# Kernel tuning notes

Hardware: AMD Instinct MI355X
Metric: run time of the kernel (lower is better)

Reference implementation:

```python
import jax, jax.numpy as jnp
import numpy as np

EMB = 1024
HEADS = 8
SEQ = 4096
LN_EPS = 1e-5


def _layernorm(x, g, b):
    mu = jnp.mean(x, axis=-1, keepdims=True)
    var = jnp.mean(jnp.square(x - mu), axis=-1, keepdims=True)
    return (x - mu) * jax.lax.rsqrt(var + LN_EPS) * g + b


def setup_inputs() -> dict:
    key = jax.random.key(0)
    ks = jax.random.split(key, 12)
    s = 1.0 / np.sqrt(EMB)
    sz = 1.0 / np.sqrt(EMB * HEADS)
    return {
        "history": jax.random.normal(ks[0], (SEQ, EMB), jnp.float32),
        "embdding": jax.random.normal(ks[1], (SEQ, EMB), jnp.float32),
        # per-head Linear weights, torch layout [out, in], stacked over heads
        "Wq_w": jax.random.uniform(ks[2], (HEADS, EMB, EMB), jnp.float32, -s, s),
        "Wq_b": jax.random.uniform(ks[3], (HEADS, EMB), jnp.float32, -s, s),
        "Wk_w": jax.random.uniform(ks[4], (HEADS, EMB, EMB), jnp.float32, -s, s),
        "Wk_b": jax.random.uniform(ks[5], (HEADS, EMB), jnp.float32, -s, s),
        "Wv_w": jax.random.uniform(ks[6], (HEADS, EMB, EMB), jnp.float32, -s, s),
        "Wv_b": jax.random.uniform(ks[7], (HEADS, EMB), jnp.float32, -s, s),
        "Wz_w": jax.random.uniform(ks[8], (EMB, EMB * HEADS), jnp.float32, -sz, sz),
        "Wz_b": jax.random.uniform(ks[9], (EMB,), jnp.float32, -sz, sz),
        "ln1_g": jnp.ones((EMB,), jnp.float32),
        "ln1_b": jnp.zeros((EMB,), jnp.float32),
        "Wf_w": jax.random.uniform(ks[10], (EMB, EMB), jnp.float32, -s, s),
        "Wf_b": jax.random.uniform(ks[11], (EMB,), jnp.float32, -s, s),
        "ln2_g": jnp.ones((EMB,), jnp.float32),
        "ln2_b": jnp.zeros((EMB,), jnp.float32),
    }


def reference(history, embdding, Wq_w, Wq_b, Wk_w, Wk_b, Wv_w, Wv_b,
              Wz_w, Wz_b, ln1_g, ln1_b, Wf_w, Wf_b, ln2_g, ln2_b):
    S, E = embdding.shape
    H = Wq_w.shape[0]
    # per-head linears (torch: y = x @ W.T + b), batched over heads
    Q = jnp.einsum('se,hfe->hsf', embdding, Wq_w) + Wq_b[:, None, :]  # [H,S,E]
    K = jnp.einsum('se,hfe->hsf', embdding, Wk_w) + Wk_b[:, None, :]
    V = jnp.einsum('se,hfe->hsf', history, Wv_w) + Wv_b[:, None, :]
    # K^T @ Q -> [H, E, E], softmax over dim=1 of the 2D matrix == last axis here
    scores = jnp.einsum('hse,hsf->hef', K, Q) / jnp.sqrt(jnp.asarray(E, Q.dtype))
    A = jax.nn.softmax(scores, axis=-1)  # [H,E,E]
    Zh = jnp.einsum('hse,hef->hsf', V, A)  # [H,S,E]
    Z = jnp.transpose(Zh, (1, 0, 2)).reshape(S, H * E)  # cat(dim=1) in head order
    O = Z @ Wz_w.T + Wz_b  # [S,E]
    LN1 = _layernorm(O, ln1_g, ln1_b) + embdding
    FN = LN1 @ Wf_w.T + Wf_b
    LN2 = _layernorm(FN, ln2_g, ln2_b) + LN1
    return LN2
```

## Files before the change

kernel.cpp:

```cpp
#include <hip/hip_runtime.h>


constexpr int EMB = 1024;
constexpr int SEQ = 4096;
constexpr int NH  = 8;

using f32x4  = __attribute__((ext_vector_type(4))) float;
using bf16x8 = __attribute__((ext_vector_type(8))) __bf16;
using us8    = __attribute__((ext_vector_type(8))) unsigned short;
using us4    = __attribute__((ext_vector_type(4))) unsigned short;

#define GLOAD_LDS16(g, l) __builtin_amdgcn_global_load_lds(                 \
    (const __attribute__((address_space(1))) void*)(g),                     \
    (__attribute__((address_space(3))) void*)(l), 16, 0, 0)

__device__ inline unsigned short f2bf(float x) {
  unsigned int u = __float_as_uint(x);
  u += 0x7FFFu + ((u >> 16) & 1u);
  return (unsigned short)(u >> 16);
}
__device__ inline float bf2f(unsigned short h) {
  return __uint_as_float(((unsigned int)h) << 16);
}
__device__ inline f32x4 ntl4(const float* p) {
  return __builtin_nontemporal_load((const f32x4*)p);
}
__device__ inline us4 cvt4(f32x4 x) {
  us4 o; o[0] = f2bf(x[0]); o[1] = f2bf(x[1]); o[2] = f2bf(x[2]); o[3] = f2bf(x[3]);
  return o;
}

template <int MODE>
__device__ __attribute__((always_inline)) void gemm_body(
    unsigned short* lds, int bx, int by, int z,
    const unsigned short* A, const unsigned short* B, void* Cout,
    int K, int lda, int ldb, int ldc,
    long long aZ, long long bZ, long long cZ,
    const float* e0, const float* e1, const float* e2, const float* e3,
    float* mpart, float* spart) {
  A += (size_t)z * aZ;
  B += (size_t)z * bZ;
  const int tid = threadIdx.x;
  const int lane = tid & 63, wid = tid >> 6;
  const int wm = wid >> 1, wn = wid & 1;
  const int row0 = bx * 64, col0 = by * 128;

  unsigned short* As = lds;
  unsigned short* Bs = lds + 64 * 64;

  f32x4 acc[2][4] = {};
  const int lrow = lane & 15, kg = lane >> 4;
  const int lr = lane >> 3;
  const int lc = (lane & 7) * 8;

  const int nt = K >> 6;
  for (int t = 0; t < nt; ++t) {
    const int k0 = t << 6;
#pragma unroll
    for (int c = 0; c < 2; ++c) {
      int chunk = wid * 2 + c;
      int r = chunk * 8 + lr;
      GLOAD_LDS16(A + (size_t)(row0 + r) * lda + k0 + lc, &As[chunk * 512]);
    }
#pragma unroll
    for (int c = 0; c < 4; ++c) {
      int chunk = wid * 4 + c;
      int r = chunk * 8 + lr;
      GLOAD_LDS16(B + (size_t)(col0 + r) * ldb + k0 + lc, &Bs[chunk * 512]);
    }
    __syncthreads();
#pragma unroll
    for (int ks = 0; ks < 2; ++ks) {
      bf16x8 a[2], b[4];
      int koff = ks * 32 + kg * 8;
#pragma unroll
      for (int i = 0; i < 2; ++i)
        a[i] = *(const bf16x8*)&As[(wm * 32 + i * 16 + lrow) * 64 + koff];
#pragma unroll
      for (int j = 0; j < 4; ++j)
        b[j] = *(const bf16x8*)&Bs[(wn * 64 + j * 16 + lrow) * 64 + koff];
#pragma unroll
      for (int i = 0; i < 2; ++i)
#pragma unroll
        for (int j = 0; j < 4; ++j)
          acc[i][j] = __builtin_amdgcn_mfma_f32_16x16x32_bf16(a[i], b[j], acc[i][j], 0, 0, 0);
    }
    __syncthreads();
  }

  const int rb = (lane >> 4) * 4, cc = lane & 15;
  unsigned short* Cs = lds;
#pragma unroll
  for (int i = 0; i < 2; ++i) {
#pragma unroll
    for (int j = 0; j < 4; ++j) {
#pragma unroll
      for (int r = 0; r < 4; ++r) {
        float val = acc[i][j][r];
        int mm = wm * 32 + i * 16 + rb + r;
        int nn = wn * 64 + j * 16 + cc;
        if (MODE == 4) {
          int m = row0 + mm, n = col0 + nn;
          float bq = e0[z * EMB + m], uu = e1[z * EMB + n];
          float bk = e2[z * EMB + n], vv = e3[z * EMB + m];
          val = (val + bq * (uu + (float)SEQ * bk) + vv * bk) * (1.0f / 32.0f);
        } else if (MODE == 5) {
          val += e0[col0 + nn];
        }
        Cs[mm * 128 + nn] = f2bf(val);
      }
    }
  }
  __syncthreads();
  unsigned short* Cg = (unsigned short*)Cout + (size_t)z * cZ;
#pragma unroll
  for (int p = 0; p < 4; ++p) {
    int idx = p * 256 + tid;
    int row = idx >> 4, col = (idx & 15) * 8;
    *(us8*)(Cg + (size_t)(row0 + row) * ldc + col0 + col) =
        *(const us8*)&Cs[row * 128 + col];
  }
  if (MODE == 2) {
#pragma unroll
    for (int p = 0; p < 4; ++p) {
      int idx = p * 256 + tid;
      int rr = idx >> 3;
      int cg = (idx & 7) * 8;
      us8 o;
#pragma unroll
      for (int e = 0; e < 8; ++e) o[e] = Cs[(cg + e) * 128 + rr];
      *(us8*)(Cg + (size_t)(col0 + rr) * ldc + row0 + cg) = o;
    }
  }
  if (MODE == 4) {
    int colx = tid >> 1, half = tid & 1;
    float mx = -1e30f;
#pragma unroll 8
    for (int r = 0; r < 32; ++r)
      mx = fmaxf(mx, bf2f(Cs[(half * 32 + r) * 128 + colx]));
    mx = fmaxf(mx, __shfl_xor(mx, 1));
    float se = 0.f;
#pragma unroll 8
    for (int r = 0; r < 32; ++r)
      se += __expf(bf2f(Cs[(half * 32 + r) * 128 + colx]) - mx);
    se += __shfl_xor(se, 1);
    if (half == 0) {
      size_t soff = ((size_t)z * 16 + bx) * EMB + col0 + colx;
      mpart[soff] = mx;
      spart[soff] = se;
    }
  }
}

template <int MODE>
__global__ __launch_bounds__(256) void gemm_nt(const unsigned short* __restrict__ A,
                                               const unsigned short* __restrict__ B,
                                               void* __restrict__ Cout,
                                               int K, int lda, int ldb, int ldc,
                                               long long aZ, long long bZ, long long cZ,
                                               int nx, int ny,
                                               const float* __restrict__ e0,
                                               const float* __restrict__ e1,
                                               const float* __restrict__ e2,
                                               const float* __restrict__ e3,
                                               float* __restrict__ mpart,
                                               float* __restrict__ spart) {
  __shared__ __align__(16) unsigned short lds[(64 + 128) * 64];
  const int q = gridDim.x >> 3;
  const int wg = (blockIdx.x & 7) * q + (blockIdx.x >> 3);
  const int bx = wg % nx, by = (wg / nx) % ny, z = wg / (nx * ny);
  gemm_body<MODE>(lds, bx, by, z, A, B, Cout, K, lda, ldb, ldc, aZ, bZ, cZ,
                  e0, e1, e2, e3, mpart, spart);
}

__global__ __launch_bounds__(256) void colsum_xt_k(const float* __restrict__ emb,
                                                   const float* __restrict__ Wv,
                                                   float* __restrict__ part,
                                                   unsigned short* __restrict__ XT,
                                                   unsigned short* __restrict__ WvT) {
  __shared__ float tileT[64][65];
  const int b = blockIdx.x, tid = threadIdx.x;
  if (b < 128) {
    int e = (b & 3) * 256 + tid;
    int y = b >> 2;
    float s = 0.f;
    for (int r = y * 128; r < y * 128 + 128; ++r) s += emb[(size_t)r * EMB + e];
    part[y * EMB + e] = s;
    return;
  }
  const float* src; unsigned short* dst; int R, r0, c0;
  if (b < 1152) {
    int tb = b - 128;
    src = emb; dst = XT; R = SEQ;
    r0 = (tb >> 4) * 64; c0 = (tb & 15) * 64;
  } else {
    int t2 = b - 1152, z = t2 >> 8, tt = t2 & 255;
    src = Wv + (size_t)z * EMB * EMB; dst = WvT + (size_t)z * EMB * EMB;
    R = EMB;
    r0 = (tt >> 4) * 64; c0 = (tt & 15) * 64;
  }
  int tx = tid & 15, ty = tid >> 4;
#pragma unroll
  for (int p = 0; p < 4; ++p) {
    int ir = p * 16 + ty;
    f32x4 x = ntl4(src + (size_t)(r0 + ir) * EMB + c0 + tx * 4);
    tileT[tx * 4 + 0][ir] = x[0]; tileT[tx * 4 + 1][ir] = x[1];
    tileT[tx * 4 + 2][ir] = x[2]; tileT[tx * 4 + 3][ir] = x[3];
  }
  __syncthreads();
#pragma unroll
  for (int p = 0; p < 4; ++p) {
    int orow = p * 16 + ty;
    f32x4 x;
    x[0] = tileT[orow][tx * 4 + 0]; x[1] = tileT[orow][tx * 4 + 1];
    x[2] = tileT[orow][tx * 4 + 2]; x[3] = tileT[orow][tx * 4 + 3];
    *(us4*)(dst + (size_t)(c0 + orow) * R + r0 + tx * 4) = cvt4(x);
  }
}

__global__ __launch_bounds__(256) void colsum_red_k(const float* __restrict__ part,
                                                    float* __restrict__ xbar) {
  int e = blockIdx.x * 256 + threadIdx.x;
  float s = 0.f;
  for (int y = 0; y < 32; ++y) s += part[y * EMB + e];
  xbar[e] = s;
}

__global__ __launch_bounds__(256) void gram_cvt_k(
    const unsigned short* __restrict__ XT, unsigned short* __restrict__ Gp,
    const float* __restrict__ Wk, const float* __restrict__ Wq,
    const float* __restrict__ hist, const float* __restrict__ Wz,
    const float* __restrict__ Wf, const float* __restrict__ xbar,
    unsigned short* __restrict__ Wkb, unsigned short* __restrict__ Wqb,
    unsigned short* __restrict__ Yb, unsigned short* __restrict__ Wzb,
    unsigned short* __restrict__ Wfb,
    float* __restrict__ u, float* __restrict__ v) {
  __shared__ __align__(16) unsigned short smem[(64 + 128) * 64];
  const int tid = threadIdx.x;
  if (blockIdx.x < 576) {
    const int wg = ((int)blockIdx.x & 7) * 72 + ((int)blockIdx.x >> 3);
    const int t = wg % 72, z = wg / 72;
    int by = 0, st = 0;
#pragma unroll
    for (int b = 7; b >= 1; --b) {
      int sb = 16 * b - b * (b - 1);
      if (t >= sb && by == 0) { by = b; st = sb; }
    }
    int bx = 2 * by + (t - st);
    gemm_body<2>(smem, bx, by, z, XT, XT, Gp, 512, SEQ, SEQ, EMB,
                 512, 512, (long long)EMB * EMB,
                 nullptr, nullptr, nullptr, nullptr, nullptr, nullptr);
    return;
  }
  int c = blockIdx.x - 576;
  if (c < 4096) {
    int gw = c * 4 + (tid >> 6);
    int lane = tid & 63;
    const float* src = (gw < 8192) ? Wk : Wq;
    unsigned short* dst = (gw < 8192) ? Wkb : Wqb;
    float* dot = (gw < 8192) ? u : v;
    int row = gw & 8191;
    const float* sr = src + (size_t)row * EMB;
    const float4* xb4 = (const float4*)xbar;
    unsigned short* dr = dst + (size_t)row * EMB;
    float s = 0.f;
#pragma unroll
    for (int j = 0; j < 4; ++j) {
      int idx = j * 64 + lane;
      f32x4 x = ntl4(sr + idx * 4);
      float4 xb = xb4[idx];
      *(us4*)(dr + idx * 4) = cvt4(x);
      s += x[0] * xb.x + x[1] * xb.y + x[2] * xb.z + x[3] * xb.w;
    }
#pragma unroll
    for (int off = 32; off; off >>= 1) s += __shfl_down(s, off);
    if (lane == 0) dot[row] = s;
  } else {
    size_t f0 = (size_t)(c - 4096) * 8192;
    const float* src; unsigned short* dst; size_t loc;
    if (f0 < 4194304ull) { src = hist; dst = Yb; loc = f0; }
    else if (f0 < 12582912ull) { src = Wz; dst = Wzb; loc = f0 - 4194304ull; }
    else { src = Wf; dst = Wfb; loc = f0 - 12582912ull; }
#pragma unroll
    for (int p = 0; p < 8; ++p) {
      int i = p * 256 + tid;
      f32x4 x = ntl4(src + loc + i * 4);
      *(us4*)(dst + loc + i * 4) = cvt4(x);
    }
  }
}

__global__ __launch_bounds__(256) void mp_dvec_k(
    const unsigned short* __restrict__ Cbf, const unsigned short* __restrict__ Wzb,
    unsigned short* __restrict__ Mp,
    const float* __restrict__ bz, const float* __restrict__ cvec,
    float* __restrict__ d) {
  __shared__ __align__(16) unsigned short smem[(64 + 128) * 64];
  const int tid = threadIdx.x;
  if (blockIdx.x < 1024) {
    const int wg = ((int)blockIdx.x & 7) * 128 + ((int)blockIdx.x >> 3);
    const int bx = wg % 16, by = (wg / 16) % 8, z = wg / 128;
    gemm_body<1>(smem, bx, by, z, Cbf, Wzb, Mp, EMB, EMB, NH * EMB, EMB,
                 (long long)EMB * EMB, (long long)EMB, (long long)EMB * EMB,
                 nullptr, nullptr, nullptr, nullptr, nullptr, nullptr);
    return;
  }
  int g = blockIdx.x - 1024;
  float* sb = (float*)smem;
  const unsigned short* row = Wzb + (size_t)g * (NH * EMB);
  float s = 0.f;
#pragma unroll
  for (int p = 0; p < 4; ++p) {
    int i = p * 256 + tid;
    us8 w = ((const us8*)row)[i];
    float4 c0 = ((const float4*)cvec)[i * 2];
    float4 c1 = ((const float4*)cvec)[i * 2 + 1];
    s += bf2f(w[0]) * c0.x + bf2f(w[1]) * c0.y + bf2f(w[2]) * c0.z + bf2f(w[3]) * c0.w;
    s += bf2f(w[4]) * c1.x + bf2f(w[5]) * c1.y + bf2f(w[6]) * c1.z + bf2f(w[7]) * c1.w;
  }
  int lane = tid & 63, w = tid >> 6;
#pragma unroll
  for (int off = 32; off; off >>= 1) s += __shfl_down(s, off);
  if (lane == 0) sb[w] = s;
  __syncthreads();
  if (tid == 0) d[g] = bz[g] + sb[0] + sb[1] + sb[2] + sb[3];
}

__global__ __launch_bounds__(256) void mred_tr_k(const unsigned short* __restrict__ Mp,
                                                 unsigned short* __restrict__ MT) {
  __shared__ float t[32][33];
  int g0 = blockIdx.x * 32, e0 = blockIdx.y * 32;
  int tx = threadIdx.x & 31, ty = threadIdx.x >> 5;
#pragma unroll
  for (int k = 0; k < 4; ++k) {
    int e = e0 + ty + k * 8;
    float s = 0.f;
#pragma unroll
    for (int h = 0; h < NH; ++h)
      s += bf2f(Mp[((size_t)h << 20) + (size_t)e * EMB + g0 + tx]);
    t[ty + k * 8][tx] = s;
  }
  __syncthreads();
#pragma unroll
  for (int k = 0; k < 4; ++k) {
    int r = ty + k * 8;
    MT[(size_t)(g0 + r) * EMB + e0 + tx] = f2bf(t[tx][r]);
  }
}

__global__ __launch_bounds__(256) void gram_red_k(const unsigned short* __restrict__ Gp,
                                                  unsigned short* __restrict__ Gbf) {
  int i = blockIdx.x * 256 + threadIdx.x;
  float4 s = {0.f, 0.f, 0.f, 0.f};
#pragma unroll
  for (int z = 0; z < 8; ++z) {
    ushort4 v = ((const ushort4*)(Gp + (size_t)z * EMB * EMB))[i];
    s.x += bf2f(v.x); s.y += bf2f(v.y); s.z += bf2f(v.z); s.w += bf2f(v.w);
  }
  ushort4 o; o.x = f2bf(s.x); o.y = f2bf(s.y); o.z = f2bf(s.z); o.w = f2bf(s.w);
  ((ushort4*)Gbf)[i] = o;
}

__global__ __launch_bounds__(256) void colstat2_k(const float* __restrict__ m_part,
                                                  const float* __restrict__ s_part,
                                                  float* __restrict__ mfin,
                                                  float* __restrict__ isfin) {
  int i = blockIdx.x * 256 + threadIdx.x;
  int h = i >> 10, col = i & 1023;
  float M = -1e30f, S = 0.f;
#pragma unroll
  for (int c = 0; c < 16; ++c) {
    float m = m_part[((size_t)h * 16 + c) * EMB + col];
    float s = s_part[((size_t)h * 16 + c) * EMB + col];
    float nm = fmaxf(M, m);
    S = S * __expf(M - nm) + s * __expf(m - nm);
    M = nm;
  }
  mfin[i] = M;
  isfin[i] = 1.0f / S;
}

__global__ __launch_bounds__(256) void at_cvec_k(const unsigned short* __restrict__ ScT,
                                                 const float* __restrict__ mfin,
                                                 const float* __restrict__ isfin,
                                                 const float* __restrict__ bv,
                                                 unsigned short* __restrict__ AT,
                                                 float* __restrict__ cbuf) {
  __shared__ float sb[4];
  int f = blockIdx.x, h = blockIdx.y, tid = threadIdx.x;
  size_t rowoff = ((size_t)h * EMB + f) * EMB;
  ushort4 xr = ((const ushort4*)(ScT + rowoff))[tid];
  float4 m  = ((const float4*)(mfin + (size_t)h * EMB))[tid];
  float4 is = ((const float4*)(isfin + (size_t)h * EMB))[tid];
  float4 b  = ((const float4*)(bv + (size_t)h * EMB))[tid];
  float a0 = __expf(bf2f(xr.x) - m.x) * is.x;
  float a1 = __expf(bf2f(xr.y) - m.y) * is.y;
  float a2 = __expf(bf2f(xr.z) - m.z) * is.z;
  float a3 = __expf(bf2f(xr.w) - m.w) * is.w;
  ushort4 o; o.x = f2bf(a0); o.y = f2bf(a1); o.z = f2bf(a2); o.w = f2bf(a3);
  ((ushort4*)(AT + rowoff))[tid] = o;
  float s = a0 * b.x + a1 * b.y + a2 * b.z + a3 * b.w;
  int lane = tid & 63, w = tid >> 6;
#pragma unroll
  for (int off = 32; off; off >>= 1) s += __shfl_down(s, off);
  if (lane == 0) sb[w] = s;
  __syncthreads();
  if (tid == 0) cbuf[h * EMB + f] = sb[0] + sb[1] + sb[2] + sb[3];
}

__global__ __launch_bounds__(256) void layernorm_k(const unsigned short* __restrict__ Xin,
                                                   const float* __restrict__ resid,
                                                   const float* __restrict__ gw,
                                                   const float* __restrict__ bw,
                                                   float* __restrict__ outf,
                                                   unsigned short* __restrict__ outb) {
  __shared__ float sb[16];
  int row = blockIdx.x, tid = threadIdx.x;
  ushort4 xr = ((const ushort4*)(Xin + (size_t)row * EMB))[tid];
  float v0 = bf2f(xr.x), v1 = bf2f(xr.y), v2 = bf2f(xr.z), v3 = bf2f(xr.w);
  float s = v0 + v1 + v2 + v3;
  float q = v0 * v0 + v1 * v1 + v2 * v2 + v3 * v3;
  int lane = tid & 63, w = tid >> 6;
#pragma unroll
  for (int off = 32; off; off >>= 1) { s += __shfl_down(s, off); q += __shfl_down(q, off); }
  if (lane == 0) { sb[w] = s; sb[8 + w] = q; }
  __syncthreads();
  float mu  = (sb[0] + sb[1] + sb[2] + sb[3]) * (1.0f / EMB);
  float var = (sb[8] + sb[9] + sb[10] + sb[11]) * (1.0f / EMB) - mu * mu;
  float rs = rsqrtf(var + 1e-5f);
  float4 rv = ((const float4*)(resid + (size_t)row * EMB))[tid];
  float4 gv = ((const float4*)gw)[tid];
  float4 bv = ((const float4*)bw)[tid];
  float o0 = (v0 - mu) * rs * gv.x + bv.x + rv.x;
  float o1 = (v1 - mu) * rs * gv.y + bv.y + rv.y;
  float o2 = (v2 - mu) * rs * gv.z + bv.z + rv.z;
  float o3 = (v3 - mu) * rs * gv.w + bv.w + rv.w;
  float4 ov; ov.x = o0; ov.y = o1; ov.z = o2; ov.w = o3;
  ((float4*)(outf + (size_t)row * EMB))[tid] = ov;
  if (outb) {
    ushort4 ob; ob.x = f2bf(o0); ob.y = f2bf(o1); ob.z = f2bf(o2); ob.w = f2bf(o3);
    ((ushort4*)(outb + (size_t)row * EMB))[tid] = ob;
  }
}

extern "C" void kernel_launch(void* const* d_in, const int* in_sizes, int n_in,
                              void* d_out, int out_size, void* d_ws, size_t ws_size,
                              hipStream_t stream) {
  const float* history = (const float*)d_in[0];
  const float* emb     = (const float*)d_in[1];
  const float* Wq_w = (const float*)d_in[2];
  const float* Wq_b = (const float*)d_in[3];
  const float* Wk_w = (const float*)d_in[4];
  const float* Wk_b = (const float*)d_in[5];
  const float* Wv_w = (const float*)d_in[6];
  const float* Wv_b = (const float*)d_in[7];
  const float* Wz_w = (const float*)d_in[8];
  const float* Wz_b = (const float*)d_in[9];
  const float* ln1_g = (const float*)d_in[10];
  const float* ln1_b = (const float*)d_in[11];
  const float* Wf_w = (const float*)d_in[12];
  const float* Wf_b = (const float*)d_in[13];
  const float* ln2_g = (const float*)d_in[14];
  const float* ln2_b = (const float*)d_in[15];

  char* ws = (char*)d_ws;
  const size_t MB = 1024ull * 1024ull;
  unsigned short* XT  = (unsigned short*)(ws + 0);
  unsigned short* Ybf = (unsigned short*)(ws + 8 * MB);
  unsigned short* Wkb = (unsigned short*)(ws + 16 * MB);
  unsigned short* Wqb = (unsigned short*)(ws + 32 * MB);
  unsigned short* WvT = (unsigned short*)(ws + 48 * MB);
  unsigned short* Wzb = (unsigned short*)(ws + 64 * MB);
  unsigned short* Wfb = (unsigned short*)(ws + 80 * MB);
  unsigned short* Gbf = (unsigned short*)(ws + 82 * MB);
  float* xpart = (float*)(ws + 84 * MB);
  float* xbar  = (float*)(ws + 84 * MB + 160 * 1024);
  float* ubuf  = (float*)(ws + 84 * MB + 192 * 1024);
  float* vbuf  = (float*)(ws + 84 * MB + 256 * 1024);
  float* cbuf  = (float*)(ws + 84 * MB + 320 * 1024);
  float* dbuf  = (float*)(ws + 84 * MB + 384 * 1024);
  unsigned short* Tbf = (unsigned short*)(ws + 85 * MB);
  float* Sc  = (float*)(ws + 101 * MB);
  char*  St  = ws + 133 * MB;
  unsigned short* ATb = (unsigned short*)(ws + 149 * MB);
  unsigned short* MTb = (unsigned short*)(ws + 165 * MB);
  float* m_part = (float*)(St);
  float* s_part = (float*)(St + 512 * 1024);
  float* mfin   = (float*)(St + 1024 * 1024);
  float* isfin  = (float*)(St + 1056 * 1024);
  unsigned short* Gp  = (unsigned short*)Sc;
  unsigned short* ScT = (unsigned short*)Sc;
  unsigned short* Cbf = Tbf;
  unsigned short* Mp  = (unsigned short*)Sc;
  unsigned short* Obf = (unsigned short*)St;
  float* LN1  = (float*)ATb;
  unsigned short* LN1b = XT;
  unsigned short* FNbf = Tbf;
  const long long EE = (long long)EMB * EMB;

  colsum_xt_k<<<dim3(3200), 256, 0, stream>>>(emb, Wv_w, xpart, XT, WvT);
  colsum_red_k<<<dim3(4), 256, 0, stream>>>(xpart, xbar);

  gram_cvt_k<<<dim3(6336), 256, 0, stream>>>(XT, Gp,
                                             Wk_w, Wq_w, history, Wz_w, Wf_w,
                                             xbar,
                                             Wkb, Wqb, Ybf, Wzb, Wfb,
                                             ubuf, vbuf);
  gram_red_k<<<dim3(EMB * EMB / 4 / 256), 256, 0, stream>>>(Gp, Gbf);
  gemm_nt<1><<<dim3(1024), 256, 0, stream>>>(Wqb, Gbf, Tbf, EMB, EMB, EMB, EMB,
                                             EE, 0, EE, 16, 8,
                                             nullptr, nullptr, nullptr, nullptr,
                                             nullptr, nullptr);
  gemm_nt<4><<<dim3(1024), 256, 0, stream>>>(Tbf, Wkb, ScT, EMB, EMB, EMB, EMB,
                                             EE, EE, EE, 16, 8,
                                             Wq_b, ubuf, Wk_b, vbuf,
                                             m_part, s_part);
  colstat2_k<<<dim3(32), 256, 0, stream>>>(m_part, s_part, mfin, isfin);
  at_cvec_k<<<dim3(EMB, NH), 256, 0, stream>>>(ScT, mfin, isfin, Wv_b, ATb, cbuf);
  gemm_nt<1><<<dim3(1024), 256, 0, stream>>>(WvT, ATb, Cbf, EMB, EMB, EMB, EMB,
                                             EE, EE, EE, 16, 8,
                                             nullptr, nullptr, nullptr, nullptr,
                                             nullptr, nullptr);
  mp_dvec_k<<<dim3(2048), 256, 0, stream>>>(Cbf, Wzb, Mp, Wz_b, cbuf, dbuf);
  mred_tr_k<<<dim3(EMB / 32, EMB / 32), 256, 0, stream>>>(Mp, MTb);
  gemm_nt<5><<<dim3(512), 256, 0, stream>>>(Ybf, MTb, Obf, EMB, EMB, EMB, EMB,
                                            0, 0, 0, 64, 8,
                                            dbuf, nullptr, nullptr, nullptr,
                                            nullptr, nullptr);
  layernorm_k<<<dim3(SEQ), 256, 0, stream>>>(Obf, emb, ln1_g, ln1_b, LN1, LN1b);
  gemm_nt<5><<<dim3(512), 256, 0, stream>>>(LN1b, Wfb, FNbf, EMB, EMB, EMB, EMB,
                                            0, 0, 0, 64, 8,
                                            Wf_b, nullptr, nullptr, nullptr,
                                            nullptr, nullptr);
  layernorm_k<<<dim3(SEQ), 256, 0, stream>>>(FNbf, LN1, ln2_g, ln2_b, (float*)d_out, nullptr);
}
```

Baseline: 269.4 us.

## Drop split-K for Gram GEMM and compute Mp transposed to avoid transpose pass

The Gram matrix GEMM over the 4096-long sequence is no longer split eight ways along K. Each of the 72 upper-triangle tiles now runs the full K loop and writes bf16 output directly, which removes the partial buffer and the gram reduction kernel. The per-head Wz·C GEMM swaps its operands so it emits the transposed product. That lets a simple plane-sum kernel replace the strided reduce-and-transpose kernel. The cost is only 72 long-running workgroups for the Gram GEMM, far fewer than the CUs available, though they overlap with the conversion blocks in the same launch.

Result: slower. 295.3 us (+9.6%).

```diff
diff --git a/kernel.cpp b/kernel.cpp
--- a/kernel.cpp
+++ b/kernel.cpp
@@ -227,7 +227,7 @@
 }
 
 __global__ __launch_bounds__(256) void gram_cvt_k(
-    const unsigned short* __restrict__ XT, unsigned short* __restrict__ Gp,
+    const unsigned short* __restrict__ XT, unsigned short* __restrict__ Gbf,
     const float* __restrict__ Wk, const float* __restrict__ Wq,
     const float* __restrict__ hist, const float* __restrict__ Wz,
     const float* __restrict__ Wf, const float* __restrict__ xbar,
@@ -237,9 +237,8 @@
     float* __restrict__ u, float* __restrict__ v) {
   __shared__ __align__(16) unsigned short smem[(64 + 128) * 64];
   const int tid = threadIdx.x;
-  if (blockIdx.x < 576) {
-    const int wg = ((int)blockIdx.x & 7) * 72 + ((int)blockIdx.x >> 3);
-    const int t = wg % 72, z = wg / 72;
+  if (blockIdx.x < 72) {
+    const int t = ((int)blockIdx.x & 7) * 9 + ((int)blockIdx.x >> 3);
     int by = 0, st = 0;
 #pragma unroll
     for (int b = 7; b >= 1; --b) {
@@ -247,12 +246,12 @@
       if (t >= sb && by == 0) { by = b; st = sb; }
     }
     int bx = 2 * by + (t - st);
-    gemm_body<2>(smem, bx, by, z, XT, XT, Gp, 512, SEQ, SEQ, EMB,
-                 512, 512, (long long)EMB * EMB,
+    gemm_body<2>(smem, bx, by, 0, XT, XT, Gbf, SEQ, SEQ, SEQ, EMB,
+                 0, 0, 0,
                  nullptr, nullptr, nullptr, nullptr, nullptr, nullptr);
     return;
   }
-  int c = blockIdx.x - 576;
+  int c = blockIdx.x - 72;
   if (c < 4096) {
     int gw = c * 4 + (tid >> 6);
     int lane = tid & 63;
@@ -292,7 +291,7 @@
 
 __global__ __launch_bounds__(256) void mp_dvec_k(
     const unsigned short* __restrict__ Cbf, const unsigned short* __restrict__ Wzb,
-    unsigned short* __restrict__ Mp,
+    unsigned short* __restrict__ MpT,
     const float* __restrict__ bz, const float* __restrict__ cvec,
     float* __restrict__ d) {
   __shared__ __align__(16) unsigned short smem[(64 + 128) * 64];
@@ -300,8 +299,8 @@
   if (blockIdx.x < 1024) {
     const int wg = ((int)blockIdx.x & 7) * 128 + ((int)blockIdx.x >> 3);
     const int bx = wg % 16, by = (wg / 16) % 8, z = wg / 128;
-    gemm_body<1>(smem, bx, by, z, Cbf, Wzb, Mp, EMB, EMB, NH * EMB, EMB,
-                 (long long)EMB * EMB, (long long)EMB, (long long)EMB * EMB,
+    gemm_body<1>(smem, bx, by, z, Wzb, Cbf, MpT, EMB, NH * EMB, EMB, EMB,
+                 (long long)EMB, (long long)EMB * EMB, (long long)EMB * EMB,
                  nullptr, nullptr, nullptr, nullptr, nullptr, nullptr);
     return;
   }
@@ -326,39 +325,17 @@
   if (tid == 0) d[g] = bz[g] + sb[0] + sb[1] + sb[2] + sb[3];
 }
 
-__global__ __launch_bounds__(256) void mred_tr_k(const unsigned short* __restrict__ Mp,
-                                                 unsigned short* __restrict__ MT) {
-  __shared__ float t[32][33];
-  int g0 = blockIdx.x * 32, e0 = blockIdx.y * 32;
-  int tx = threadIdx.x & 31, ty = threadIdx.x >> 5;
-#pragma unroll
-  for (int k = 0; k < 4; ++k) {
-    int e = e0 + ty + k * 8;
-    float s = 0.f;
-#pragma unroll
-    for (int h = 0; h < NH; ++h)
-      s += bf2f(Mp[((size_t)h << 20) + (size_t)e * EMB + g0 + tx]);
-    t[ty + k * 8][tx] = s;
-  }
-  __syncthreads();
-#pragma unroll
-  for (int k = 0; k < 4; ++k) {
-    int r = ty + k * 8;
-    MT[(size_t)(g0 + r) * EMB + e0 + tx] = f2bf(t[tx][r]);
-  }
-}
-
-__global__ __launch_bounds__(256) void gram_red_k(const unsigned short* __restrict__ Gp,
-                                                  unsigned short* __restrict__ Gbf) {
+__global__ __launch_bounds__(256) void plane_red_k(const unsigned short* __restrict__ in,
+                                                   unsigned short* __restrict__ out) {
   int i = blockIdx.x * 256 + threadIdx.x;
   float4 s = {0.f, 0.f, 0.f, 0.f};
 #pragma unroll
   for (int z = 0; z < 8; ++z) {
-    ushort4 v = ((const ushort4*)(Gp + (size_t)z * EMB * EMB))[i];
+    ushort4 v = ((const ushort4*)(in + (size_t)z * EMB * EMB))[i];
     s.x += bf2f(v.x); s.y += bf2f(v.y); s.z += bf2f(v.z); s.w += bf2f(v.w);
   }
   ushort4 o; o.x = f2bf(s.x); o.y = f2bf(s.y); o.z = f2bf(s.z); o.w = f2bf(s.w);
-  ((ushort4*)Gbf)[i] = o;
+  ((ushort4*)out)[i] = o;
 }
 
 __global__ __launch_bounds__(256) void colstat2_k(const float* __restrict__ m_part,
@@ -488,10 +465,9 @@
   float* s_part = (float*)(St + 512 * 1024);
   float* mfin   = (float*)(St + 1024 * 1024);
   float* isfin  = (float*)(St + 1056 * 1024);
-  unsigned short* Gp  = (unsigned short*)Sc;
   unsigned short* ScT = (unsigned short*)Sc;
   unsigned short* Cbf = Tbf;
-  unsigned short* Mp  = (unsigned short*)Sc;
+  unsigned short* MpT = (unsigned short*)Sc;
   unsigned short* Obf = (unsigned short*)St;
   float* LN1  = (float*)ATb;
   unsigned short* LN1b = XT;
@@ -501,12 +477,11 @@
   colsum_xt_k<<<dim3(3200), 256, 0, stream>>>(emb, Wv_w, xpart, XT, WvT);
   colsum_red_k<<<dim3(4), 256, 0, stream>>>(xpart, xbar);
 
-  gram_cvt_k<<<dim3(6336), 256, 0, stream>>>(XT, Gp,
+  gram_cvt_k<<<dim3(5832), 256, 0, stream>>>(XT, Gbf,
                                              Wk_w, Wq_w, history, Wz_w, Wf_w,
                                              xbar,
                                              Wkb, Wqb, Ybf, Wzb, Wfb,
                                              ubuf, vbuf);
-  gram_red_k<<<dim3(EMB * EMB / 4 / 256), 256, 0, stream>>>(Gp, Gbf);
   gemm_nt<1><<<dim3(1024), 256, 0, stream>>>(Wqb, Gbf, Tbf, EMB, EMB, EMB, EMB,
                                              EE, 0, EE, 16, 8,
                                              nullptr, nullptr, nullptr, nullptr,
@@ -521,8 +496,8 @@
                                              EE, EE, EE, 16, 8,
                                              nullptr, nullptr, nullptr, nullptr,
                                              nullptr, nullptr);
-  mp_dvec_k<<<dim3(2048), 256, 0, stream>>>(Cbf, Wzb, Mp, Wz_b, cbuf, dbuf);
-  mred_tr_k<<<dim3(EMB / 32, EMB / 32), 256, 0, stream>>>(Mp, MTb);
+  mp_dvec_k<<<dim3(2048), 256, 0, stream>>>(Cbf, Wzb, MpT, Wz_b, cbuf, dbuf);
+  plane_red_k<<<dim3(EMB * EMB / 4 / 256), 256, 0, stream>>>(MpT, MTb);
   gemm_nt<5><<<dim3(512), 256, 0, stream>>>(Ybf, MTb, Obf, EMB, EMB, EMB, EMB,
                                             0, 0, 0, 64, 8,
                                             dbuf, nullptr, nullptr, nullptr,
```
